# Kernel tuning notes

Hardware: AMD Instinct MI355X
Metric: run time of the kernel (lower is better)

Reference implementation:

```python
import jax, jax.numpy as jnp
import numpy as np

FEAT = 1024   # feat_dim
EMB = 64      # emb_dim
GROUP = 16    # group == fc_dim
DG = FEAT // GROUP  # 64, per-group query/key dim and conv out channels per group
R = 1024      # num_rois
N = 1024      # nongt_dim


def setup_inputs() -> dict:
    key = jax.random.key(0)
    ks = jax.random.split(key, 8)
    inp = {
        "position_embedding": jax.random.normal(ks[0], (R, N, EMB), dtype=jnp.float32),
        "roi_feat": jax.random.normal(ks[1], (R, FEAT), dtype=jnp.float32),
        # fc_q / fc_k: Linear(feat_dim, feat_dim)
        "Wq": jax.random.normal(ks[2], (FEAT, FEAT), dtype=jnp.float32) * 0.02,
        "bq": jnp.zeros((FEAT,), dtype=jnp.float32),
        "Wk": jax.random.normal(ks[3], (FEAT, FEAT), dtype=jnp.float32) * 0.02,
        "bk": jnp.zeros((FEAT,), dtype=jnp.float32),
        # fc_pos_feat: Linear(emb_dim, fc_dim=group)
        "Wp": jax.random.normal(ks[4], (GROUP, EMB), dtype=jnp.float32) * 0.1,
        "bp": jnp.zeros((GROUP,), dtype=jnp.float32),
        # conv_cat: Conv2d(group*feat_dim, feat_dim, k=1, groups=group)
        # per group g: in FEAT channels -> out DG channels. Shape [GROUP, DG, FEAT].
        "Wc": jax.random.normal(ks[5], (GROUP, DG, FEAT), dtype=jnp.float32) * 0.02,
        "bc": jnp.zeros((FEAT,), dtype=jnp.float32),
        "nongt_dim": N,
    }
    return inp


def reference(position_embedding, roi_feat, Wq, bq, Wk, bk, Wp, bp, Wc, bc, nongt_dim):
    scale = 1.0 / np.sqrt(float(DG))
    # fc_pos_feat + relu -> aff_weight [R, GROUP, N]
    pos_feat = jax.nn.relu(jnp.einsum("rne,ge->rng", position_embedding, Wp) + bp)
    aff_weight = jnp.transpose(pos_feat, (0, 2, 1))  # [R, GROUP, N]
    nongt = roi_feat[:nongt_dim]                     # [N, FEAT]
    q = (roi_feat @ Wq.T + bq).reshape(-1, GROUP, DG)   # [R, GROUP, DG]
    k = (nongt @ Wk.T + bk).reshape(-1, GROUP, DG)      # [N, GROUP, DG]
    # per-group QK^T with log position bias
    aff = jnp.einsum("rgd,ngd->rgn", q, k) * scale      # [R, GROUP, N]
    weighted = jnp.log(jnp.clip(aff_weight, 1e-6, None)) + aff
    att = jax.nn.softmax(weighted, axis=2)              # [R, GROUP, N]
    # attention * V -> [R, GROUP, FEAT]
    out_t = jnp.einsum("rgn,nf->rgf", att, nongt)
    # grouped 1x1 conv combine: group g maps FEAT -> DG output channels
    out = jnp.einsum("rgf,gof->rgo", out_t, Wc).reshape(-1, FEAT) + bc
    return out
```

## Files before the change

### kernel.cpp

```cpp
#include <hip/hip_runtime.h>

#define R_DIM 1024
#define N_DIM 1024
#define FEAT  1024
#define EMB   64
#define GROUP 16
#define DG    64

typedef _Float16 half8  __attribute__((ext_vector_type(8)));
typedef _Float16 half4v __attribute__((ext_vector_type(4)));
typedef float    f32x4  __attribute__((ext_vector_type(4)));

__device__ __forceinline__ half8 cvt8(const float* p) {
  const float4 a = *(const float4*)p;
  const float4 b = *(const float4*)(p + 4);
  half8 h;
  h[0] = (_Float16)a.x; h[1] = (_Float16)a.y; h[2] = (_Float16)a.z; h[3] = (_Float16)a.w;
  h[4] = (_Float16)b.x; h[5] = (_Float16)b.y; h[6] = (_Float16)b.z; h[7] = (_Float16)b.w;
  return h;
}

__global__ __launch_bounds__(256) void qk_gemm(
    const float* __restrict__ roi, const float* __restrict__ Wq,
    const float* __restrict__ bq,  const float* __restrict__ Wk,
    const float* __restrict__ bk,  _Float16* __restrict__ qh,
    _Float16* __restrict__ khI)
{
  __shared__ float aT[16][68];
  __shared__ float bqT[16][68];
  __shared__ float bkT[16][68];
  const int t  = threadIdx.x;
  const int r0 = blockIdx.x * 64, c0 = blockIdx.y * 64;
  const int lr = t >> 2, lk = (t & 3) << 2;
  const int ty = t >> 4, tx = t & 15;
  const float* ap  = roi + (r0 + lr) * FEAT + lk;
  const float* bqp = Wq  + (c0 + lr) * FEAT + lk;
  const float* bkp = Wk  + (c0 + lr) * FEAT + lk;
  float4 av  = *(const float4*)ap;
  float4 bqv = *(const float4*)bqp;
  float4 bkv = *(const float4*)bkp;
  float accq[4][4] = {}, acck[4][4] = {};
  for (int k0 = 0; k0 < FEAT; k0 += 16) {
    aT[lk+0][lr]=av.x;   aT[lk+1][lr]=av.y;   aT[lk+2][lr]=av.z;   aT[lk+3][lr]=av.w;
    bqT[lk+0][lr]=bqv.x; bqT[lk+1][lr]=bqv.y; bqT[lk+2][lr]=bqv.z; bqT[lk+3][lr]=bqv.w;
    bkT[lk+0][lr]=bkv.x; bkT[lk+1][lr]=bkv.y; bkT[lk+2][lr]=bkv.z; bkT[lk+3][lr]=bkv.w;
    __syncthreads();
    const bool more = (k0 + 16) < FEAT;
    float4 av_n, bqv_n, bkv_n;
    if (more) {
      av_n  = *(const float4*)(ap  + k0 + 16);
      bqv_n = *(const float4*)(bqp + k0 + 16);
      bkv_n = *(const float4*)(bkp + k0 + 16);
    }
#pragma unroll
    for (int kk = 0; kk < 16; ++kk) {
      const float4 a4 = *(const float4*)&aT[kk][ty << 2];
      const float4 q4 = *(const float4*)&bqT[kk][tx << 2];
      const float4 k4 = *(const float4*)&bkT[kk][tx << 2];
      const float ar[4] = {a4.x, a4.y, a4.z, a4.w};
      const float qr[4] = {q4.x, q4.y, q4.z, q4.w};
      const float kr[4] = {k4.x, k4.y, k4.z, k4.w};
#pragma unroll
      for (int i = 0; i < 4; ++i)
#pragma unroll
        for (int j = 0; j < 4; ++j) {
          accq[i][j] += ar[i] * qr[j];
          acck[i][j] += ar[i] * kr[j];
        }
    }
    __syncthreads();
    if (more) { av = av_n; bqv = bqv_n; bkv = bkv_n; }
  }
  const float4 bq4 = *(const float4*)(bq + c0 + (tx << 2));
  const float4 bk4 = *(const float4*)(bk + c0 + (tx << 2));
  const float bqr[4] = {bq4.x, bq4.y, bq4.z, bq4.w};
  const float bkr[4] = {bk4.x, bk4.y, bk4.z, bk4.w};
  const int g  = c0 >> 6;
#pragma unroll
  for (int i = 0; i < 4; ++i) {
    half4v oq, ok;
#pragma unroll
    for (int j = 0; j < 4; ++j) {
      oq[j] = (_Float16)(accq[i][j] + bqr[j]);
      ok[j] = (_Float16)(acck[i][j] + bkr[j]);
    }
    const int row = r0 + (ty << 2) + i;
    *(half4v*)(qh + (size_t)row * FEAT + c0 + (tx << 2)) = oq;
    *(half4v*)(khI + ((((size_t)g << 3) + (tx >> 1)) << 13) + (row << 3) + ((tx & 1) << 2)) = ok;
  }
}

__global__ __launch_bounds__(256) void pos_mfma(
    const float* __restrict__ pe, const float* __restrict__ Wp,
    const float* __restrict__ bp, _Float16* __restrict__ logw)
{
  __shared__ __align__(16) _Float16 Xs[128 * 64];
  __shared__ __align__(16) _Float16 LW[16][136];
  const int t  = threadIdx.x;
  const int bx = blockIdx.x;
  const int w = t >> 6, l = t & 63, q16 = l & 15, q4 = l >> 4;

  const float* wpp = Wp + (q16 << 6) + (q4 << 3);
  const half8 wb0 = cvt8(wpp);
  const half8 wb1 = cvt8(wpp + 32);
  const float bpg = bp[q16];

  const size_t base = ((size_t)bx) << 15;
  float4 cur[8], nxt[8];
#pragma unroll
  for (int i = 0; i < 8; ++i)
    cur[i] = *(const float4*)(pe + base + ((size_t)((i << 8) + t) << 2));

  for (int tt = 0; tt < 4; ++tt) {
    if (tt < 3) {
#pragma unroll
      for (int i = 0; i < 8; ++i)
        nxt[i] = *(const float4*)(pe + base + ((size_t)(((tt + 1) << 11) + (i << 8) + t) << 2));
    }
#pragma unroll
    for (int i = 0; i < 8; ++i) {
      const int flat4 = (i << 8) + t;
      const int row = flat4 >> 4, e4 = flat4 & 15;
      half4v h;
      h[0] = (_Float16)cur[i].x; h[1] = (_Float16)cur[i].y;
      h[2] = (_Float16)cur[i].z; h[3] = (_Float16)cur[i].w;
      const int boff = (row << 7) + ((e4 << 3) ^ ((row & 7) << 4));
      *(half4v*)((char*)Xs + boff) = h;
    }
    __syncthreads();
#pragma unroll
    for (int sub = 0; sub < 2; ++sub) {
      const int lrbase = (w << 5) + (sub << 4);
      const int lrr = lrbase + q16;
      const int b0 = (lrr << 7) + (((q4 << 4))      ^ ((lrr & 7) << 4));
      const int b1 = (lrr << 7) + (((q4 << 4) + 64) ^ ((lrr & 7) << 4));
      const half8 a0 = *(const half8*)((const char*)Xs + b0);
      const half8 a1 = *(const half8*)((const char*)Xs + b1);
      f32x4 acc = (f32x4){0.f, 0.f, 0.f, 0.f};
      acc = __builtin_amdgcn_mfma_f32_16x16x32_f16(a0, wb0, acc, 0, 0, 0);
      acc = __builtin_amdgcn_mfma_f32_16x16x32_f16(a1, wb1, acc, 0, 0, 0);
      half4v o;
#pragma unroll
      for (int j = 0; j < 4; ++j) {
        const float v = fmaxf(acc[j] + bpg, 1e-6f);
        o[j] = (_Float16)__logf(v);
      }
      *(half4v*)&LW[q16][lrbase + (q4 << 2)] = o;
    }
    __syncthreads();
    const int rowblk = (bx << 2) + tt;
    const int r = rowblk >> 3, n0 = (rowblk & 7) << 7;
    const int gg = t >> 4, n4 = t & 15;
    const half8 vv = *(const half8*)&LW[gg][n4 << 3];
    *(half8*)(logw + ((size_t)((r << 4) + gg) << 10) + n0 + (n4 << 3)) = vv;
    if (tt < 3) {
#pragma unroll
      for (int i = 0; i < 8; ++i) cur[i] = nxt[i];
    }
  }
}

__global__ __launch_bounds__(256) void kc_gemm(
    const float* __restrict__ roi, const float* __restrict__ Wc,
    _Float16* __restrict__ kctI)
{
  __shared__ float aT[16][68];
  __shared__ float bT[16][68];
  const int t   = threadIdx.x;
  const int n0g = blockIdx.x * 64;
  const int g   = blockIdx.y;
  const int lr = t >> 2, lk = (t & 3) << 2;
  const int ty = t >> 4, tx = t & 15;
  const float* ap  = Wc  + (size_t)(g * DG + lr) * FEAT + lk;
  const float* bp_ = roi + (size_t)(n0g + lr) * FEAT + lk;
  float4 av = *(const float4*)ap;
  float4 bv = *(const float4*)bp_;
  float acc[4][4] = {};
  for (int k0 = 0; k0 < FEAT; k0 += 16) {
    aT[lk+0][lr]=av.x; aT[lk+1][lr]=av.y; aT[lk+2][lr]=av.z; aT[lk+3][lr]=av.w;
    bT[lk+0][lr]=bv.x; bT[lk+1][lr]=bv.y; bT[lk+2][lr]=bv.z; bT[lk+3][lr]=bv.w;
    __syncthreads();
    const bool more = (k0 + 16) < FEAT;
    float4 av_n, bv_n;
    if (more) {
      av_n = *(const float4*)(ap  + k0 + 16);
      bv_n = *(const float4*)(bp_ + k0 + 16);
    }
#pragma unroll
    for (int kk = 0; kk < 16; ++kk) {
      const float4 a4 = *(const float4*)&aT[kk][ty << 2];
      const float4 b4 = *(const float4*)&bT[kk][tx << 2];
      const float ar[4] = {a4.x, a4.y, a4.z, a4.w};
      const float br[4] = {b4.x, b4.y, b4.z, b4.w};
#pragma unroll
      for (int i = 0; i < 4; ++i)
#pragma unroll
        for (int j = 0; j < 4; ++j) acc[i][j] += ar[i] * br[j];
    }
    __syncthreads();
    if (more) { av = av_n; bv = bv_n; }
  }
#pragma unroll
  for (int i = 0; i < 4; ++i) {
    half4v o4;
#pragma unroll
    for (int j = 0; j < 4; ++j) o4[j] = (_Float16)acc[i][j];
    *(half4v*)(kctI + ((((size_t)g << 7) + ((n0g + (tx << 2)) >> 3)) << 9)
               + (((ty << 2) + i) << 3) + ((tx & 1) << 2)) = o4;
  }
}

__global__ __launch_bounds__(256) void attn_mfma(
    const _Float16* __restrict__ qh, const _Float16* __restrict__ khI,
    const _Float16* __restrict__ logw, const _Float16* __restrict__ kctI,
    const float* __restrict__ bc, float* __restrict__ outp)
{
  __shared__ float Ored[4][16][68];
  __shared__ float redm[4][16];
  __shared__ float redl[4][16];
#define PLD 1032
  __shared__ __align__(16) _Float16 P[16][PLD];

  const int t   = threadIdx.x;
  const int w   = t >> 6;
  const int l   = t & 63;
  const int q16 = l & 15;
  const int q4  = l >> 4;
  const int bid = blockIdx.x;
  const int g   = (bid & 7) + ((bid >> 9) << 3);
  const int r0  = ((bid >> 3) & 63) << 4;
  const int nbase = w << 8;

  const half8* qp = (const half8*)(qh + (size_t)(r0 + q16) * FEAT + (g << 6) + (q4 << 3));
  const half8 a0 = qp[0];
  const half8 a1 = qp[4];

  const _Float16* kbase = khI  + ((size_t)g << 16);
  const _Float16* cbase = kctI + ((size_t)g << 16);

  f32x4 S[16];
#pragma unroll
  for (int i = 0; i < 16; ++i) S[i] = (f32x4){0.f, 0.f, 0.f, 0.f};
#pragma unroll
  for (int t16 = 0; t16 < 16; ++t16) {
    const int n = nbase + (t16 << 4) + q16;
    const half8 k0 = *(const half8*)(kbase + ((size_t)q4 << 13) + (n << 3));
    const half8 k1 = *(const half8*)(kbase + ((size_t)(4 + q4) << 13) + (n << 3));
    S[t16] = __builtin_amdgcn_mfma_f32_16x16x32_f16(a0, k0, S[t16], 0, 0, 0);
    S[t16] = __builtin_amdgcn_mfma_f32_16x16x32_f16(a1, k1, S[t16], 0, 0, 0);
  }

#pragma unroll
  for (int t16 = 0; t16 < 16; ++t16) {
    const int n = nbase + (t16 << 4) + q16;
#pragma unroll
    for (int j = 0; j < 4; ++j) {
      const int r = r0 + (q4 << 2) + j;
      const float lw = (float)logw[(size_t)(((r << 4) + g) << 10) + n];
      S[t16][j] = S[t16][j] * 0.125f + lw;
    }
  }

  float m[4] = {-1e30f, -1e30f, -1e30f, -1e30f};
#pragma unroll
  for (int t16 = 0; t16 < 16; ++t16)
#pragma unroll
    for (int j = 0; j < 4; ++j) m[j] = fmaxf(m[j], S[t16][j]);
#pragma unroll
  for (int off = 8; off; off >>= 1)
#pragma unroll
    for (int j = 0; j < 4; ++j) m[j] = fmaxf(m[j], __shfl_xor(m[j], off));
  if (q16 == 0) {
#pragma unroll
    for (int j = 0; j < 4; ++j) redm[w][(q4 << 2) + j] = m[j];
  }
  __syncthreads();
#pragma unroll
  for (int j = 0; j < 4; ++j) {
    const int r = (q4 << 2) + j;
    m[j] = fmaxf(fmaxf(redm[0][r], redm[1][r]), fmaxf(redm[2][r], redm[3][r]));
  }

  float ls[4] = {0.f, 0.f, 0.f, 0.f};
#pragma unroll
  for (int t16 = 0; t16 < 16; ++t16) {
    const int n = nbase + (t16 << 4) + q16;
#pragma unroll
    for (int j = 0; j < 4; ++j) {
      const float p = __expf(S[t16][j] - m[j]);
      ls[j] += p;
      P[(q4 << 2) + j][n] = (_Float16)p;
    }
  }
#pragma unroll
  for (int off = 8; off; off >>= 1)
#pragma unroll
    for (int j = 0; j < 4; ++j) ls[j] += __shfl_xor(ls[j], off);
  if (q16 == 0) {
#pragma unroll
    for (int j = 0; j < 4; ++j) redl[w][(q4 << 2) + j] = ls[j];
  }
  __syncthreads();

  f32x4 O[4];
#pragma unroll
  for (int ot = 0; ot < 4; ++ot) O[ot] = (f32x4){0.f, 0.f, 0.f, 0.f};
#pragma unroll
  for (int ks = 0; ks < 8; ++ks) {
    const int nk = nbase + (ks << 5) + (q4 << 3);
    const half8 pa = *(const half8*)&P[q16][nk];
#pragma unroll
    for (int ot = 0; ot < 4; ++ot) {
      const half8 bfr = *(const half8*)(cbase + ((size_t)(nk >> 3) << 9) + (((ot << 4) + q16) << 3));
      O[ot] = __builtin_amdgcn_mfma_f32_16x16x32_f16(pa, bfr, O[ot], 0, 0, 0);
    }
  }
#pragma unroll
  for (int ot = 0; ot < 4; ++ot)
#pragma unroll
    for (int j = 0; j < 4; ++j)
      Ored[w][(q4 << 2) + j][(ot << 4) + q16] = O[ot][j];
  __syncthreads();

  const int r  = t >> 4;
  const int o0 = (t & 15) << 2;
  const float lsum = redl[0][r] + redl[1][r] + redl[2][r] + redl[3][r];
  const float inv  = 1.0f / lsum;
  float o[4];
#pragma unroll
  for (int c = 0; c < 4; ++c)
    o[c] = Ored[0][r][o0 + c] + Ored[1][r][o0 + c] + Ored[2][r][o0 + c] + Ored[3][r][o0 + c];
  const float4 bcv = *(const float4*)(bc + (g << 6) + o0);
  float4 res;
  res.x = o[0] * inv + bcv.x;
  res.y = o[1] * inv + bcv.y;
  res.z = o[2] * inv + bcv.z;
  res.w = o[3] * inv + bcv.w;
  *(float4*)(outp + (size_t)(r0 + r) * FEAT + (g << 6) + o0) = res;
}

extern "C" void kernel_launch(void* const* d_in, const int* in_sizes, int n_in,
                              void* d_out, int out_size, void* d_ws, size_t ws_size,
                              hipStream_t stream)
{
  const float* pe  = (const float*)d_in[0];
  const float* roi = (const float*)d_in[1];
  const float* Wq  = (const float*)d_in[2];
  const float* bq  = (const float*)d_in[3];
  const float* Wk  = (const float*)d_in[4];
  const float* bk  = (const float*)d_in[5];
  const float* Wp  = (const float*)d_in[6];
  const float* bp  = (const float*)d_in[7];
  const float* Wc  = (const float*)d_in[8];
  const float* bc  = (const float*)d_in[9];
  float* outp = (float*)d_out;

  char* ws = (char*)d_ws;
  _Float16* qh   = (_Float16*)(ws);
  _Float16* khI  = (_Float16*)(ws + ((size_t)2 << 20));
  _Float16* kctI = (_Float16*)(ws + ((size_t)4 << 20));
  _Float16* logw = (_Float16*)(ws + ((size_t)6 << 20));

  qk_gemm<<<dim3(16, 16), 256, 0, stream>>>(roi, Wq, bq, Wk, bk, qh, khI);
  pos_mfma<<<2048, 256, 0, stream>>>(pe, Wp, bp, logw);
  kc_gemm<<<dim3(16, 16), 256, 0, stream>>>(roi, Wc, kctI);
  attn_mfma<<<1024, 256, 0, stream>>>(qh, khI, logw, kctI, bc, outp);
}
```

Before: 190.4 us.

## Load pos-embedding directly into MFMA registers and transpose QK MFMA for vector logw reads

pos_mfma drops its LDS staging and two barriers per tile. Each wave loads position-embedding rows straight into MFMA operand registers and writes log-weights directly to global memory. Q is now stored in the same interleaved per-group layout as K, and attn_mfma swaps the MFMA operands so each lane holds one row across four keys. That lets logw be read as half4 vectors, P be written as half4, and the row max and sum reductions shrink to two cross-lane shuffles. The aim is to cut LDS traffic and syncs in pos_mfma and scalar, strided logw loads in attention, at the cost of less coalesced global writes from pos_mfma.

```diff
diff --git a/kernel.cpp b/kernel.cpp
--- a/kernel.cpp
+++ b/kernel.cpp
@@ -19,11 +19,17 @@
   h[4] = (_Float16)b.x; h[5] = (_Float16)b.y; h[6] = (_Float16)b.z; h[7] = (_Float16)b.w;
   return h;
 }
+__device__ __forceinline__ half8 cvt8v(float4 a, float4 b) {
+  half8 h;
+  h[0] = (_Float16)a.x; h[1] = (_Float16)a.y; h[2] = (_Float16)a.z; h[3] = (_Float16)a.w;
+  h[4] = (_Float16)b.x; h[5] = (_Float16)b.y; h[6] = (_Float16)b.z; h[7] = (_Float16)b.w;
+  return h;
+}
 
 __global__ __launch_bounds__(256) void qk_gemm(
     const float* __restrict__ roi, const float* __restrict__ Wq,
     const float* __restrict__ bq,  const float* __restrict__ Wk,
-    const float* __restrict__ bk,  _Float16* __restrict__ qh,
+    const float* __restrict__ bk,  _Float16* __restrict__ qhI,
     _Float16* __restrict__ khI)
 {
   __shared__ float aT[16][68];
@@ -75,7 +81,7 @@
   const float4 bk4 = *(const float4*)(bk + c0 + (tx << 2));
   const float bqr[4] = {bq4.x, bq4.y, bq4.z, bq4.w};
   const float bkr[4] = {bk4.x, bk4.y, bk4.z, bk4.w};
-  const int g  = c0 >> 6;
+  const int g = c0 >> 6;
 #pragma unroll
   for (int i = 0; i < 4; ++i) {
     half4v oq, ok;
@@ -85,8 +91,9 @@
       ok[j] = (_Float16)(acck[i][j] + bkr[j]);
     }
     const int row = r0 + (ty << 2) + i;
-    *(half4v*)(qh + (size_t)row * FEAT + c0 + (tx << 2)) = oq;
-    *(half4v*)(khI + ((((size_t)g << 3) + (tx >> 1)) << 13) + (row << 3) + ((tx & 1) << 2)) = ok;
+    const size_t idx = ((((size_t)g << 3) + (tx >> 1)) << 13) + ((size_t)row << 3) + ((tx & 1) << 2);
+    *(half4v*)(qhI + idx) = oq;
+    *(half4v*)(khI + idx) = ok;
   }
 }
 
@@ -94,69 +101,41 @@
     const float* __restrict__ pe, const float* __restrict__ Wp,
     const float* __restrict__ bp, _Float16* __restrict__ logw)
 {
-  __shared__ __align__(16) _Float16 Xs[128 * 64];
-  __shared__ __align__(16) _Float16 LW[16][136];
-  const int t  = threadIdx.x;
-  const int bx = blockIdx.x;
+  const int t = threadIdx.x;
   const int w = t >> 6, l = t & 63, q16 = l & 15, q4 = l >> 4;
-
   const float* wpp = Wp + (q16 << 6) + (q4 << 3);
   const half8 wb0 = cvt8(wpp);
   const half8 wb1 = cvt8(wpp + 32);
   const float bpg = bp[q16];
 
-  const size_t base = ((size_t)bx) << 15;
-  float4 cur[8], nxt[8];
-#pragma unroll
-  for (int i = 0; i < 8; ++i)
-    cur[i] = *(const float4*)(pe + base + ((size_t)((i << 8) + t) << 2));
-
-  for (int tt = 0; tt < 4; ++tt) {
-    if (tt < 3) {
-#pragma unroll
-      for (int i = 0; i < 8; ++i)
-        nxt[i] = *(const float4*)(pe + base + ((size_t)(((tt + 1) << 11) + (i << 8) + t) << 2));
-    }
-#pragma unroll
-    for (int i = 0; i < 8; ++i) {
-      const int flat4 = (i << 8) + t;
-      const int row = flat4 >> 4, e4 = flat4 & 15;
-      half4v h;
-      h[0] = (_Float16)cur[i].x; h[1] = (_Float16)cur[i].y;
-      h[2] = (_Float16)cur[i].z; h[3] = (_Float16)cur[i].w;
-      const int boff = (row << 7) + ((e4 << 3) ^ ((row & 7) << 4));
-      *(half4v*)((char*)Xs + boff) = h;
-    }
-    __syncthreads();
-#pragma unroll
-    for (int sub = 0; sub < 2; ++sub) {
-      const int lrbase = (w << 5) + (sub << 4);
-      const int lrr = lrbase + q16;
-      const int b0 = (lrr << 7) + (((q4 << 4))      ^ ((lrr & 7) << 4));
-      const int b1 = (lrr << 7) + (((q4 << 4) + 64) ^ ((lrr & 7) << 4));
-      const half8 a0 = *(const half8*)((const char*)Xs + b0);
-      const half8 a1 = *(const half8*)((const char*)Xs + b1);
-      f32x4 acc = (f32x4){0.f, 0.f, 0.f, 0.f};
-      acc = __builtin_amdgcn_mfma_f32_16x16x32_f16(a0, wb0, acc, 0, 0, 0);
-      acc = __builtin_amdgcn_mfma_f32_16x16x32_f16(a1, wb1, acc, 0, 0, 0);
-      half4v o;
-#pragma unroll
-      for (int j = 0; j < 4; ++j) {
-        const float v = fmaxf(acc[j] + bpg, 1e-6f);
-        o[j] = (_Float16)__logf(v);
-      }
-      *(half4v*)&LW[q16][lrbase + (q4 << 2)] = o;
-    }
-    __syncthreads();
-    const int rowblk = (bx << 2) + tt;
-    const int r = rowblk >> 3, n0 = (rowblk & 7) << 7;
-    const int gg = t >> 4, n4 = t & 15;
-    const half8 vv = *(const half8*)&LW[gg][n4 << 3];
-    *(half8*)(logw + ((size_t)((r << 4) + gg) << 10) + n0 + (n4 << 3)) = vv;
-    if (tt < 3) {
-#pragma unroll
-      for (int i = 0; i < 8; ++i) cur[i] = nxt[i];
-    }
+  int tile = ((blockIdx.x << 2) + w) << 3;
+  const float* src = pe + ((size_t)tile << 10) + (q16 << 6) + (q4 << 3);
+  float4 c0 = *(const float4*)(src);
+  float4 c1 = *(const float4*)(src + 4);
+  float4 c2 = *(const float4*)(src + 32);
+  float4 c3 = *(const float4*)(src + 36);
+  for (int it = 0; it < 8; ++it, ++tile) {
+    float4 n0 = c0, n1 = c1, n2 = c2, n3 = c3;
+    if (it < 7) {
+      const float* s2 = src + ((size_t)(it + 1) << 10);
+      n0 = *(const float4*)(s2);
+      n1 = *(const float4*)(s2 + 4);
+      n2 = *(const float4*)(s2 + 32);
+      n3 = *(const float4*)(s2 + 36);
+    }
+    const half8 a0 = cvt8v(c0, c1);
+    const half8 a1 = cvt8v(c2, c3);
+    f32x4 acc = (f32x4){0.f, 0.f, 0.f, 0.f};
+    acc = __builtin_amdgcn_mfma_f32_16x16x32_f16(a0, wb0, acc, 0, 0, 0);
+    acc = __builtin_amdgcn_mfma_f32_16x16x32_f16(a1, wb1, acc, 0, 0, 0);
+    half4v o;
+#pragma unroll
+    for (int j = 0; j < 4; ++j)
+      o[j] = (_Float16)__logf(fmaxf(acc[j] + bpg, 1e-6f));
+    const int r  = tile >> 6;
+    const int nb = ((tile & 63) << 4) + (q4 << 2);
+    *(half4v*)(logw + ((((size_t)r << 4) + q16) << 10) + nb) = o;
+    c0 = n0; c1 = n1; c2 = n2; c3 = n3;
   }
 }
 
@@ -210,15 +189,15 @@
   }
 }
 
+#define PLD 1032
 __global__ __launch_bounds__(256) void attn_mfma(
-    const _Float16* __restrict__ qh, const _Float16* __restrict__ khI,
+    const _Float16* __restrict__ qhI, const _Float16* __restrict__ khI,
     const _Float16* __restrict__ logw, const _Float16* __restrict__ kctI,
     const float* __restrict__ bc, float* __restrict__ outp)
 {
   __shared__ float Ored[4][16][68];
   __shared__ float redm[4][16];
   __shared__ float redl[4][16];
-#define PLD 1032
   __shared__ __align__(16) _Float16 P[16][PLD];
 
   const int t   = threadIdx.x;
@@ -231,12 +210,12 @@
   const int r0  = ((bid >> 3) & 63) << 4;
   const int nbase = w << 8;
 
-  const half8* qp = (const half8*)(qh + (size_t)(r0 + q16) * FEAT + (g << 6) + (q4 << 3));
-  const half8 a0 = qp[0];
-  const half8 a1 = qp[4];
-
   const _Float16* kbase = khI  + ((size_t)g << 16);
+  const _Float16* qbase = qhI  + ((size_t)g << 16);
   const _Float16* cbase = kctI + ((size_t)g << 16);
+
+  const half8 b0 = *(const half8*)(qbase + ((size_t)q4 << 13) + ((r0 + q16) << 3));
+  const half8 b1 = *(const half8*)(qbase + ((size_t)(4 + q4) << 13) + ((r0 + q16) << 3));
 
   f32x4 S[16];
 #pragma unroll
@@ -246,60 +225,44 @@
     const int n = nbase + (t16 << 4) + q16;
     const half8 k0 = *(const half8*)(kbase + ((size_t)q4 << 13) + (n << 3));
     const half8 k1 = *(const half8*)(kbase + ((size_t)(4 + q4) << 13) + (n << 3));
-    S[t16] = __builtin_amdgcn_mfma_f32_16x16x32_f16(a0, k0, S[t16], 0, 0, 0);
-    S[t16] = __builtin_amdgcn_mfma_f32_16x16x32_f16(a1, k1, S[t16], 0, 0, 0);
-  }
-
+    S[t16] = __builtin_amdgcn_mfma_f32_16x16x32_f16(k0, b0, S[t16], 0, 0, 0);
+    S[t16] = __builtin_amdgcn_mfma_f32_16x16x32_f16(k1, b1, S[t16], 0, 0, 0);
+  }
+  const _Float16* lwp = logw + ((((size_t)(r0 + q16)) << 4) + (size_t)g) * 1024;
 #pragma unroll
   for (int t16 = 0; t16 < 16; ++t16) {
-    const int n = nbase + (t16 << 4) + q16;
+    const half4v lw = *(const half4v*)(lwp + nbase + (t16 << 4) + (q4 << 2));
+#pragma unroll
+    for (int j = 0; j < 4; ++j)
+      S[t16][j] = S[t16][j] * 0.125f + (float)lw[j];
+  }
+
+  float m = -1e30f;
+#pragma unroll
+  for (int t16 = 0; t16 < 16; ++t16)
+#pragma unroll
+    for (int j = 0; j < 4; ++j) m = fmaxf(m, S[t16][j]);
+  m = fmaxf(m, __shfl_xor(m, 16));
+  m = fmaxf(m, __shfl_xor(m, 32));
+  if (q4 == 0) redm[w][q16] = m;
+  __syncthreads();
+  m = fmaxf(fmaxf(redm[0][q16], redm[1][q16]), fmaxf(redm[2][q16], redm[3][q16]));
+
+  float ls = 0.f;
+#pragma unroll
+  for (int t16 = 0; t16 < 16; ++t16) {
+    half4v pv;
 #pragma unroll
     for (int j = 0; j < 4; ++j) {
-      const int r = r0 + (q4 << 2) + j;
-      const float lw = (float)logw[(size_t)(((r << 4) + g) << 10) + n];
-      S[t16][j] = S[t16][j] * 0.125f + lw;
-    }
-  }
-
-  float m[4] = {-1e30f, -1e30f, -1e30f, -1e30f};
-#pragma unroll
-  for (int t16 = 0; t16 < 16; ++t16)
-#pragma unroll
-    for (int j = 0; j < 4; ++j) m[j] = fmaxf(m[j], S[t16][j]);
-#pragma unroll
-  for (int off = 8; off; off >>= 1)
-#pragma unroll
-    for (int j = 0; j < 4; ++j) m[j] = fmaxf(m[j], __shfl_xor(m[j], off));
-  if (q16 == 0) {
-#pragma unroll
-    for (int j = 0; j < 4; ++j) redm[w][(q4 << 2) + j] = m[j];
-  }
-  __syncthreads();
-#pragma unroll
-  for (int j = 0; j < 4; ++j) {
-    const int r = (q4 << 2) + j;
-    m[j] = fmaxf(fmaxf(redm[0][r], redm[1][r]), fmaxf(redm[2][r], redm[3][r]));
-  }
-
-  float ls[4] = {0.f, 0.f, 0.f, 0.f};
-#pragma unroll
-  for (int t16 = 0; t16 < 16; ++t16) {
-    const int n = nbase + (t16 << 4) + q16;
-#pragma unroll
-    for (int j = 0; j < 4; ++j) {
-      const float p = __expf(S[t16][j] - m[j]);
-      ls[j] += p;
-      P[(q4 << 2) + j][n] = (_Float16)p;
-    }
-  }
-#pragma unroll
-  for (int off = 8; off; off >>= 1)
-#pragma unroll
-    for (int j = 0; j < 4; ++j) ls[j] += __shfl_xor(ls[j], off);
-  if (q16 == 0) {
-#pragma unroll
-    for (int j = 0; j < 4; ++j) redl[w][(q4 << 2) + j] = ls[j];
-  }
+      const float p = __expf(S[t16][j] - m);
+      ls += p;
+      pv[j] = (_Float16)p;
+    }
+    *(half4v*)&P[q16][nbase + (t16 << 4) + (q4 << 2)] = pv;
+  }
+  ls += __shfl_xor(ls, 16);
+  ls += __shfl_xor(ls, 32);
+  if (q4 == 0) redl[w][q16] = ls;
   __syncthreads();
 
   f32x4 O[4];
@@ -356,13 +319,13 @@
   float* outp = (float*)d_out;
 
   char* ws = (char*)d_ws;
-  _Float16* qh   = (_Float16*)(ws);
+  _Float16* qhI  = (_Float16*)(ws);
   _Float16* khI  = (_Float16*)(ws + ((size_t)2 << 20));
   _Float16* kctI = (_Float16*)(ws + ((size_t)4 << 20));
   _Float16* logw = (_Float16*)(ws + ((size_t)6 << 20));
 
-  qk_gemm<<<dim3(16, 16), 256, 0, stream>>>(roi, Wq, bq, Wk, bk, qh, khI);
+  qk_gemm<<<dim3(16, 16), 256, 0, stream>>>(roi, Wq, bq, Wk, bk, qhI, khI);
   pos_mfma<<<2048, 256, 0, stream>>>(pe, Wp, bp, logw);
   kc_gemm<<<dim3(16, 16), 256, 0, stream>>>(roi, Wc, kctI);
-  attn_mfma<<<1024, 256, 0, stream>>>(qh, khI, logw, kctI, bc, outp);
-}
+  attn_mfma<<<1024, 256, 0, stream>>>(qhI, khI, logw, kctI, bc, outp);
+}
```

Measured after the change: 192.3 us. Within noise of the previous version (+1.0%).
